# Kernel optimization log

Measured on AMD Instinct MI355X. Metric: run time of the kernel, lower is better.

The kernel has to match this reference:

```python
import jax, jax.numpy as jnp
import numpy as np

N = 30000      # nodes
NNZ = 480000   # edges (avg degree 16)
D_IN, D_H, D_OUT = 64, 256, 128


def spmm(rows, cols, vals, feat, n):
    # (sparse [n,n] in COO) @ feat : out[r] += vals[e] * feat[cols[e]]
    return jax.ops.segment_sum(vals[:, None] * feat[cols], rows, num_segments=n)


def graph_inception(l_feat, r_feat, rows, cols, vals, W1, b1, W2, b2):
    # hop=1, eval mode (F.dropout with training=False is identity)
    n = l_feat.shape[0]
    x0 = r_feat  # dropout(Korder_list[r][0])
    x1 = l_feat  # dropout(Korder_list[l][0])
    # network_l @ x0 and network_r (=transpose) @ x1
    l_K = spmm(rows, cols, vals, x0, n)          # [N, D]
    r_K = spmm(cols, rows, vals, x1, n)          # [N, D]
    l_re = l_K @ W1 + b1                          # weight1(l_Korder)
    r_re = r_K @ W1 + b1
    # Multiply: mm(network, a) * b then weight2 (mm result equals l_K / r_K)
    l_mul = (l_K * x1) @ W2 + b2
    r_mul = (r_K * x0) @ W2 + b2
    return l_re + l_mul, r_re + r_mul


def setup_inputs() -> dict:
    key = jax.random.key(0)
    ks = jax.random.split(key, 9)
    l_feat = jax.random.normal(ks[0], (N, D_IN), jnp.float32)
    r_feat = jax.random.normal(ks[1], (N, D_IN), jnp.float32)
    edge_rows = jax.random.randint(ks[2], (NNZ,), 0, N, jnp.int32)
    edge_cols = jax.random.randint(ks[3], (NNZ,), 0, N, jnp.int32)
    edge_vals = jax.random.uniform(ks[4], (NNZ,), jnp.float32)
    W1 = jax.random.normal(ks[5], (D_IN, D_H), jnp.float32) / np.sqrt(D_IN)
    W2 = jax.random.normal(ks[6], (D_IN, D_H), jnp.float32) / np.sqrt(D_IN)
    W3 = jax.random.normal(ks[7], (D_H, D_OUT), jnp.float32) / np.sqrt(D_H)
    W4 = jax.random.normal(ks[8], (D_H, D_OUT), jnp.float32) / np.sqrt(D_H)
    return {
        "l_feat": l_feat, "r_feat": r_feat,
        "edge_rows": edge_rows, "edge_cols": edge_cols, "edge_vals": edge_vals,
        "W1": W1, "b1": jnp.zeros((D_H,), jnp.float32),
        "W2": W2, "b2": jnp.zeros((D_H,), jnp.float32),
        "W3": W3, "b3": jnp.zeros((D_OUT,), jnp.float32),
        "W4": W4, "b4": jnp.zeros((D_OUT,), jnp.float32),
    }


def reference(l_feat, r_feat, edge_rows, edge_cols, edge_vals,
              W1, b1, W2, b2, W3, b3, W4, b4):
    a1, b1_ = graph_inception(l_feat, r_feat, edge_rows, edge_cols, edge_vals, W1, b1, W2, b2)
    y1 = jax.nn.relu(a1)
    z1 = jax.nn.relu(b1_)
    a2, _ = graph_inception(y1, z1, edge_rows, edge_cols, edge_vals, W3, b3, W4, b4)
    return jax.nn.relu(a2)  # [N, 128]
```

## Files before the change

### kernel.cpp

```cpp
#include <hip/hip_runtime.h>

#define NN     30000
#define NNZE   480000
#define NPART  8
#define PROWS  (NN / NPART)
#define NCHUNK 32
#define CH_E   (NNZE / NCHUNK)
#define QBIN   7500
#define SCB    118

using s8 = __attribute__((ext_vector_type(8))) short;
using f4 = __attribute__((ext_vector_type(4))) float;

__device__ __forceinline__ unsigned short f2bf(float x) {
    unsigned int u = __float_as_uint(x);
    u += 0x7fff + ((u >> 16) & 1);
    return (unsigned short)(u >> 16);
}
__device__ __forceinline__ float bf2f(unsigned short h) {
    return __uint_as_float(((unsigned int)h) << 16);
}
__device__ __forceinline__ float bflo(unsigned int z) {
    return __uint_as_float(z << 16);
}
__device__ __forceinline__ float bfhi(unsigned int z) {
    return __uint_as_float(z & 0xffff0000u);
}
__device__ __forceinline__ int2 nt_pair(const int2* p) {
    long long v = __builtin_nontemporal_load((const long long*)p);
    int2 r; r.x = (int)(unsigned int)v; r.y = (int)(v >> 32); return r;
}
__device__ __forceinline__ unsigned long long nt_u64(const void* p) {
    return __builtin_nontemporal_load((const unsigned long long*)p);
}

#define FEAT4   (NN * 64 / 4)
#define PREP_W0 (2 * FEAT4)
#define PREP_W1 (PREP_W0 + 98688)
__global__ __launch_bounds__(256) void prep_kernel(
    const float* __restrict__ lf, const float* __restrict__ rf,
    const float* __restrict__ W1, const float* __restrict__ W2,
    const float* __restrict__ W3, const float* __restrict__ W4,
    const float* __restrict__ b1, const float* __restrict__ b2,
    const float* __restrict__ b3, const float* __restrict__ b4,
    unsigned short* __restrict__ lfb, unsigned short* __restrict__ rfb,
    unsigned short* __restrict__ Wt1, unsigned short* __restrict__ Wt2,
    float* __restrict__ bias1, float* __restrict__ bias2)
{
    int i = blockIdx.x * 256 + threadIdx.x;
    if (i < PREP_W0) {
        const float* src = (i < FEAT4) ? lf : rf;
        unsigned short* dst = (i < FEAT4) ? lfb : rfb;
        int j = (i < FEAT4) ? i : i - FEAT4;
        float4 v = ((const float4*)src)[j];
        ushort4 o;
        o.x = f2bf(v.x); o.y = f2bf(v.y); o.z = f2bf(v.z); o.w = f2bf(v.w);
        ((ushort4*)dst)[j] = o;
    } else if (i < PREP_W1) {
        int j = i - PREP_W0;
        if (j < 32768) {
            int n = j >> 7, k = j & 127;
            float v = (k < 64) ? W1[(size_t)k * 256 + n] : W2[(size_t)(k - 64) * 256 + n];
            Wt1[j] = f2bf(v);
        } else if (j < 32768 + 65536) {
            int q = j - 32768;
            int n = q >> 9, k = q & 511;
            float v = (k < 256) ? W3[(size_t)k * 128 + n] : W4[(size_t)(k - 256) * 128 + n];
            Wt2[q] = f2bf(v);
        } else if (j < 98304 + 256) {
            int n = j - 98304; bias1[n] = b1[n] + b2[n];
        } else if (j < 98560 + 128) {
            int n = j - 98560; bias2[n] = b3[n] + b4[n];
        }
    }
}

__global__ __launch_bounds__(256) void count_rank_kernel(
    const int* __restrict__ rows, const int* __restrict__ cols,
    int* __restrict__ histP,
    unsigned short* __restrict__ rank_r, unsigned short* __restrict__ rank_c)
{
    int b = blockIdx.x;
    int side    = b >> 7;
    int chunk   = (b & 127) >> 2;
    int quarter = b & 3;
    const int* keys = side ? cols : rows;
    unsigned short* rank = side ? rank_c : rank_r;
    int binlo = quarter * QBIN;

    __shared__ int h[QBIN];
    for (int i = threadIdx.x; i < QBIN; i += 256) h[i] = 0;
    __syncthreads();

    int e0 = chunk * CH_E;
    for (int e = e0 + threadIdx.x; e < e0 + CH_E; e += 256) {
        int k = __builtin_nontemporal_load(keys + e) - binlo;
        if ((unsigned)k < (unsigned)QBIN)
            rank[e] = (unsigned short)atomicAdd(&h[k], 1);
    }
    __syncthreads();

    int* dst = histP + ((size_t)(side * NCHUNK + chunk)) * NN + binlo;
    for (int i = threadIdx.x; i < QBIN; i += 256)
        __builtin_nontemporal_store(h[i], dst + i);
}

__global__ __launch_bounds__(256) void scanP_kernel(
    int* __restrict__ histP,
    int* __restrict__ rp, int* __restrict__ cp, int* __restrict__ totals)
{
    int b = blockIdx.x;
    int side = (b >= SCB) ? 1 : 0;
    int lb = side ? b - SCB : b;
    int t = threadIdx.x;
    int bin = lb * 256 + t;

    int run = 0;
    if (bin < NN) {
        int* base = histP + (size_t)side * NCHUNK * NN + bin;
#pragma unroll 4
        for (int c = 0; c < NCHUNK; ++c) {
            int v = base[(size_t)c * NN];
            base[(size_t)c * NN] = run;
            run += v;
        }
    }
    __shared__ int s[256];
    s[t] = run;
    __syncthreads();
#pragma unroll
    for (int off = 1; off < 256; off <<= 1) {
        int u = (t >= off) ? s[t - off] : 0;
        __syncthreads();
        s[t] += u;
        __syncthreads();
    }
    if (bin < NN) (side ? cp : rp)[bin] = s[t] - run;
    if (t == 255) totals[b] = s[t];
}

__global__ __launch_bounds__(256) void scan_addtot_kernel(
    int* __restrict__ rp, int* __restrict__ cp, const int* __restrict__ totals)
{
    int b = blockIdx.x;
    int side = (b >= SCB) ? 1 : 0;
    int lb = side ? b - SCB : b;
    int t = threadIdx.x;

    __shared__ int s[128];
    if (t < 128) s[t] = (t < SCB) ? totals[side * SCB + t] : 0;
    __syncthreads();
#pragma unroll
    for (int off = 1; off < 128; off <<= 1) {
        int u = 0;
        if (t < 128 && t >= off) u = s[t - off];
        __syncthreads();
        if (t < 128) s[t] += u;
        __syncthreads();
    }
    int off = (lb == 0) ? 0 : s[lb - 1];
    int idx = lb * 256 + t;
    int* ptr = side ? cp : rp;
    if (idx < NN) ptr[idx] += off;
    if (b == 0   && t == 0) rp[NN] = NNZE;
    if (b == SCB && t == 0) cp[NN] = NNZE;
}

__global__ __launch_bounds__(256) void scatter_rank_kernel(
    const int* __restrict__ rows, const int* __restrict__ cols,
    const float* __restrict__ vals,
    const unsigned short* __restrict__ rank_r, const unsigned short* __restrict__ rank_c,
    const int* __restrict__ histP,
    const int* __restrict__ rp, const int* __restrict__ cp,
    int2* __restrict__ csr_pair, int2* __restrict__ csc_pair)
{
    int part = blockIdx.x & (NPART - 1);
    int lo = part * PROWS, hi = lo + PROWS;
    int nb = gridDim.x >> 3;
    int bj = blockIdx.x >> 3;
    int stride = nb * 256;
    for (int e = bj * 256 + threadIdx.x; e < NNZE; e += stride) {
        int r = __builtin_nontemporal_load(rows + e);
        int c = __builtin_nontemporal_load(cols + e);
        float fv = __builtin_nontemporal_load(vals + e);
        int vb = __float_as_int(fv);
        int chunk = e / CH_E;
        if (r >= lo && r < hi) {
            int p = rp[r] + histP[(size_t)chunk * NN + r]
                  + (int)__builtin_nontemporal_load(rank_r + e);
            csr_pair[p] = make_int2(c, vb);
        }
        if (c >= lo && c < hi) {
            int q = cp[c] + histP[(size_t)(NCHUNK + chunk) * NN + c]
                  + (int)__builtin_nontemporal_load(rank_c + e);
            csc_pair[q] = make_int2(r, vb);
        }
    }
}

#define G64CAP 768
__global__ __launch_bounds__(256) void gather64_x_kernel(
    const int* __restrict__ rp, const int2* __restrict__ rpair,
    const int* __restrict__ cp, const int2* __restrict__ cpair,
    const unsigned short* __restrict__ lfb, const unsigned short* __restrict__ rfb,
    unsigned short* __restrict__ X1, unsigned short* __restrict__ X2)
{
    int side = blockIdx.y;
    const int*  ptr  = side ? cp    : rp;
    const int2* pair = side ? cpair : rpair;
    const unsigned int* gf = (const unsigned int*)(side ? lfb : rfb);
    const unsigned int* mf = (const unsigned int*)(side ? rfb : lfb);
    unsigned int* X = (unsigned int*)(side ? X2 : X1);

    __shared__ int2 sp[G64CAP];
    int w0 = blockIdx.x * 8;
    int e0b = ptr[w0];
    int nseg = ptr[w0 + 8] - e0b;
    for (int i = threadIdx.x; i < nseg && i < G64CAP; i += 256)
        sp[i] = nt_pair(&pair[e0b + i]);
    __syncthreads();

    int w = w0 + (threadIdx.x >> 5);
    int l = threadIdx.x & 31;
    int ea = ptr[w] - e0b, eb = ptr[w + 1] - e0b;
    float a0 = 0.f, a1 = 0.f;
    int e = ea;
    for (; e + 7 < eb; e += 8) {
        int2 p[8];
#pragma unroll
        for (int j = 0; j < 8; ++j)
            p[j] = (e + j < G64CAP) ? sp[e + j] : nt_pair(&pair[e0b + e + j]);
        unsigned int z[8];
#pragma unroll
        for (int j = 0; j < 8; ++j) z[j] = gf[(size_t)p[j].x * 32 + l];
#pragma unroll
        for (int j = 0; j < 8; ++j) {
            float v = __int_as_float(p[j].y);
            a0 += v * bflo(z[j]);
            a1 += v * bfhi(z[j]);
        }
    }
    for (; e < eb; ++e) {
        int2 p0 = (e < G64CAP) ? sp[e] : nt_pair(&pair[e0b + e]);
        unsigned int z0 = gf[(size_t)p0.x * 32 + l];
        float v = __int_as_float(p0.y);
        a0 += v * bflo(z0);
        a1 += v * bfhi(z0);
    }
    unsigned int m = mf[(size_t)w * 32 + l];
    float m0 = a0 * bflo(m);
    float m1 = a1 * bfhi(m);
    unsigned int o0 = (unsigned int)f2bf(a0) | ((unsigned int)f2bf(a1) << 16);
    unsigned int o1 = (unsigned int)f2bf(m0) | ((unsigned int)f2bf(m1) << 16);
    __builtin_nontemporal_store(o0, &X[(size_t)w * 64 + l]);
    __builtin_nontemporal_store(o1, &X[(size_t)w * 64 + 32 + l]);
}

__global__ __launch_bounds__(256) void gather256_x_kernel(
    const int* __restrict__ ptr, const int2* __restrict__ pair,
    const unsigned short* __restrict__ z1b, const unsigned short* __restrict__ y1b,
    unsigned short* __restrict__ X3)
{
    int w    = blockIdx.x * 4 + (threadIdx.x >> 6);
    int lane = threadIdx.x & 63;
    int e0 = ptr[w], e1 = ptr[w + 1];
    const ushort4* Z = (const ushort4*)z1b;
    f4 acc = {0.f, 0.f, 0.f, 0.f};
    int e = e0;
    for (; e + 15 < e1; e += 16) {
        int2 p[16];
#pragma unroll
        for (int j = 0; j < 16; ++j) p[j] = nt_pair(&pair[e + j]);
        ushort4 z[16];
#pragma unroll
        for (int j = 0; j < 16; ++j) z[j] = Z[(size_t)p[j].x * 64 + lane];
#pragma unroll
        for (int j = 0; j < 16; ++j) {
            float v = __int_as_float(p[j].y);
            acc[0] += v * bf2f(z[j].x);
            acc[1] += v * bf2f(z[j].y);
            acc[2] += v * bf2f(z[j].z);
            acc[3] += v * bf2f(z[j].w);
        }
    }
    for (; e + 3 < e1; e += 4) {
        int2 p[4];
#pragma unroll
        for (int j = 0; j < 4; ++j) p[j] = nt_pair(&pair[e + j]);
        ushort4 z[4];
#pragma unroll
        for (int j = 0; j < 4; ++j) z[j] = Z[(size_t)p[j].x * 64 + lane];
#pragma unroll
        for (int j = 0; j < 4; ++j) {
            float v = __int_as_float(p[j].y);
            acc[0] += v * bf2f(z[j].x);
            acc[1] += v * bf2f(z[j].y);
            acc[2] += v * bf2f(z[j].z);
            acc[3] += v * bf2f(z[j].w);
        }
    }
    for (; e < e1; ++e) {
        int2 p0 = nt_pair(&pair[e]);
        float v0 = __int_as_float(p0.y);
        ushort4 z0 = Z[(size_t)p0.x * 64 + lane];
        acc[0] += v0 * bf2f(z0.x);
        acc[1] += v0 * bf2f(z0.y);
        acc[2] += v0 * bf2f(z0.z);
        acc[3] += v0 * bf2f(z0.w);
    }
    unsigned long long yu = nt_u64(&((const ushort4*)y1b)[(size_t)w * 64 + lane]);
    float y0 = bf2f((unsigned short)(yu));
    float y1 = bf2f((unsigned short)(yu >> 16));
    float y2 = bf2f((unsigned short)(yu >> 32));
    float y3 = bf2f((unsigned short)(yu >> 48));
    unsigned long long o0 =
        (unsigned long long)f2bf(acc[0])
      | ((unsigned long long)f2bf(acc[1]) << 16)
      | ((unsigned long long)f2bf(acc[2]) << 32)
      | ((unsigned long long)f2bf(acc[3]) << 48);
    unsigned long long o1 =
        (unsigned long long)f2bf(acc[0] * y0)
      | ((unsigned long long)f2bf(acc[1] * y1) << 16)
      | ((unsigned long long)f2bf(acc[2] * y2) << 32)
      | ((unsigned long long)f2bf(acc[3] * y3) << 48);
    unsigned long long* X3u = (unsigned long long*)X3;
    __builtin_nontemporal_store(o0, &X3u[(size_t)w * 128 + lane]);
    __builtin_nontemporal_store(o1, &X3u[(size_t)w * 128 + 64 + lane]);
}

template<int K, int DOUT, bool OUT_BF16, bool NT_A, bool NT_B>
__global__ __launch_bounds__(256) void mfma_gemm_kernel(
    const unsigned short* Xa, const unsigned short* Xb,
    const unsigned short* __restrict__ Wt, const float* __restrict__ bias,
    void* outa, void* outb)
{
    constexpr int WC = DOUT / 4;
    constexpr int FN = WC / 16;
    __shared__ s8 sX[64 * 8];
    __shared__ s8 sW[DOUT * 8];

    const unsigned short* X = blockIdx.y ? Xb : Xa;
    void* outv              = blockIdx.y ? outb : outa;
    const bool nt_out       = blockIdx.y ? NT_B : NT_A;

    const int t       = threadIdx.x;
    const int rowbase = blockIdx.x * 64;
    const int wid     = t >> 6;
    const int lane    = t & 63;
    const int l15     = lane & 15;
    const int kg      = lane >> 4;

    f4 acc[4][FN] = {};

    for (int kc = 0; kc < K; kc += 64) {
#pragma unroll
        for (int it = 0; it < 2; ++it) {
            int ch = t + it * 256;
            int r = ch >> 3, c = ch & 7;
            int row = rowbase + r;
            s8 v = {};
            if (row < NN)
                v = __builtin_nontemporal_load(((const s8*)X) + ((size_t)row * K + kc) / 8 + c);
            sX[(r << 3) | (c ^ (r & 7))] = v;
        }
#pragma unroll
        for (int it = 0; it < DOUT / 32; ++it) {
            int ch = t + it * 256;
            int n = ch >> 3, c = ch & 7;
            sW[(n << 3) | (c ^ (n & 7))] = ((const s8*)Wt)[((size_t)n * K + kc) / 8 + c];
        }
        __syncthreads();

#pragma unroll
        for (int ks = 0; ks < 2; ++ks) {
            int cch = ks * 4 + kg;
            s8 a[4], b[FN];
#pragma unroll
            for (int fm = 0; fm < 4; ++fm) {
                int r0 = fm * 16 + l15;
                a[fm] = sX[(r0 << 3) | (cch ^ (r0 & 7))];
            }
#pragma unroll
            for (int fn = 0; fn < FN; ++fn) {
                int n0 = wid * WC + fn * 16 + l15;
                b[fn] = sW[(n0 << 3) | (cch ^ (n0 & 7))];
            }
#pragma unroll
            for (int fm = 0; fm < 4; ++fm)
#pragma unroll
                for (int fn = 0; fn < FN; ++fn)
                    acc[fm][fn] = __builtin_amdgcn_mfma_f32_16x16x32_bf16(
                        a[fm], b[fn], acc[fm][fn], 0, 0, 0);
        }
        __syncthreads();
    }

#pragma unroll
    for (int fm = 0; fm < 4; ++fm) {
#pragma unroll
        for (int fn = 0; fn < FN; ++fn) {
            int col = wid * WC + fn * 16 + l15;
            float bv = bias[col];
#pragma unroll
            for (int j = 0; j < 4; ++j) {
                int row = rowbase + fm * 16 + kg * 4 + j;
                if (row < NN) {
                    float v = fmaxf(acc[fm][fn][j] + bv, 0.f);
                    if constexpr (OUT_BF16) {
                        unsigned short* q = (unsigned short*)outv + (size_t)row * DOUT + col;
                        if (nt_out) __builtin_nontemporal_store(f2bf(v), q);
                        else        *q = f2bf(v);
                    } else {
                        float* q = (float*)outv + (size_t)row * DOUT + col;
                        if (nt_out) __builtin_nontemporal_store(v, q);
                        else        *q = v;
                    }
                }
            }
        }
    }
}

extern "C" void kernel_launch(void* const* d_in, const int* in_sizes, int n_in,
                              void* d_out, int out_size, void* d_ws, size_t ws_size,
                              hipStream_t stream)
{
    const float* l_feat = (const float*)d_in[0];
    const float* r_feat = (const float*)d_in[1];
    const int*   rows   = (const int*)  d_in[2];
    const int*   cols   = (const int*)  d_in[3];
    const float* vals   = (const float*)d_in[4];
    const float* W1     = (const float*)d_in[5];
    const float* b1     = (const float*)d_in[6];
    const float* W2     = (const float*)d_in[7];
    const float* b2     = (const float*)d_in[8];
    const float* W3     = (const float*)d_in[9];
    const float* b3     = (const float*)d_in[10];
    const float* W4     = (const float*)d_in[11];
    const float* b4     = (const float*)d_in[12];
    float* out = (float*)d_out;

    char* p = (char*)d_ws;
    unsigned short* X1  = (unsigned short*)p; p += (size_t)NN * 128 * 2;
    unsigned short* X2  = (unsigned short*)p; p += (size_t)NN * 128 * 2;
    unsigned short* X3  = (unsigned short*)p; p += (size_t)NN * 512 * 2;
    unsigned short* z1b = (unsigned short*)p; p += (size_t)NN * 256 * 2;
    unsigned short* y1b = (unsigned short*)p; p += (size_t)NN * 256 * 2;
    unsigned short* lfb = (unsigned short*)p; p += (size_t)NN * 64 * 2;
    unsigned short* rfb = (unsigned short*)p; p += (size_t)NN * 64 * 2;
    int* histP    = (int*)p; p += (size_t)2 * NCHUNK * NN * 4;
    int* totals   = (int*)p; p += 256 * 4;
    unsigned short* Wt1 = (unsigned short*)p; p += 32768 * 2;
    unsigned short* Wt2 = (unsigned short*)p; p += 65536 * 2;
    float* bias1 = (float*)p; p += 256 * 4;
    float* bias2 = (float*)p; p += 128 * 4;
    int*   row_ptr  = (int*)p; p += (size_t)(NN + 4) * 4;
    int*   col_ptr  = (int*)p; p += (size_t)(NN + 4) * 4;
    int2*  csr_pair = (int2*)p; p += (size_t)NNZE * 8;
    int2*  csc_pair = (int2*)p; p += (size_t)NNZE * 8;
    unsigned short* rank_r = (unsigned short*)p; p += (size_t)NNZE * 2;
    unsigned short* rank_c = (unsigned short*)p; p += (size_t)NNZE * 2;

    prep_kernel<<<(PREP_W1 + 255) / 256, 256, 0, stream>>>(
        l_feat, r_feat, W1, W2, W3, W4, b1, b2, b3, b4,
        lfb, rfb, Wt1, Wt2, bias1, bias2);

    count_rank_kernel<<<256, 256, 0, stream>>>(rows, cols, histP, rank_r, rank_c);

    scanP_kernel<<<2 * SCB, 256, 0, stream>>>(histP, row_ptr, col_ptr, totals);
    scan_addtot_kernel<<<2 * SCB, 256, 0, stream>>>(row_ptr, col_ptr, totals);

    scatter_rank_kernel<<<2048, 256, 0, stream>>>(
        rows, cols, vals, rank_r, rank_c, histP, row_ptr, col_ptr, csr_pair, csc_pair);

    {
        dim3 grid(NN / 8, 2);
        gather64_x_kernel<<<grid, 256, 0, stream>>>(
            row_ptr, csr_pair, col_ptr, csc_pair, lfb, rfb, X1, X2);
    }

    {
        dim3 grid((NN + 63) / 64, 2);
        mfma_gemm_kernel<128, 256, true, true, false><<<grid, 256, 0, stream>>>(
            X1, X2, Wt1, bias1, y1b, z1b);
    }

    gather256_x_kernel<<<NN / 4, 256, 0, stream>>>(row_ptr, csr_pair, z1b, y1b, X3);

    {
        dim3 grid((NN + 63) / 64, 1);
        mfma_gemm_kernel<512, 128, false, true, true><<<grid, 256, 0, stream>>>(
            X3, X3, Wt2, bias2, out, out);
    }
}
```

Baseline: 200.3 us.

## Pack CSR edges into 32-bit index+bf16 value, merge prep with counting

Edge entries are packed as a 15-bit node index plus a bf16 edge value in one 32-bit word, halving CSR/CSC storage and gather-side index traffic. The prep and histogram-count kernels are fused into one launch, and the 256-wide gather is reworked to 32 lanes per row loading 8 bf16 values each. This risks precision loss from rounding edge values to bf16. The 15-bit index mask holds only because N=30000 fits in 32768.

New measurement: 200.8 us. About the same (+0.2%).

```diff
diff --git a/kernel.cpp b/kernel.cpp
--- a/kernel.cpp
+++ b/kernel.cpp
@@ -26,18 +26,19 @@
 __device__ __forceinline__ float bfhi(unsigned int z) {
     return __uint_as_float(z & 0xffff0000u);
 }
-__device__ __forceinline__ int2 nt_pair(const int2* p) {
-    long long v = __builtin_nontemporal_load((const long long*)p);
-    int2 r; r.x = (int)(unsigned int)v; r.y = (int)(v >> 32); return r;
-}
-__device__ __forceinline__ unsigned long long nt_u64(const void* p) {
-    return __builtin_nontemporal_load((const unsigned long long*)p);
+__device__ __forceinline__ int nt_i32(const int* p) {
+    return __builtin_nontemporal_load(p);
+}
+
+__device__ __forceinline__ unsigned int pack_iv(int idx, float v) {
+    return (unsigned int)(idx & 0x7fff) | ((unsigned int)f2bf(v) << 16);
 }
 
 #define FEAT4   (NN * 64 / 4)
 #define PREP_W0 (2 * FEAT4)
 #define PREP_W1 (PREP_W0 + 98688)
-__global__ __launch_bounds__(256) void prep_kernel(
+#define PREPB   ((PREP_W1 + 255) / 256)
+__global__ __launch_bounds__(256) void prep_count_kernel(
     const float* __restrict__ lf, const float* __restrict__ rf,
     const float* __restrict__ W1, const float* __restrict__ W2,
     const float* __restrict__ W3, const float* __restrict__ W4,
@@ -45,42 +46,44 @@
     const float* __restrict__ b3, const float* __restrict__ b4,
     unsigned short* __restrict__ lfb, unsigned short* __restrict__ rfb,
     unsigned short* __restrict__ Wt1, unsigned short* __restrict__ Wt2,
-    float* __restrict__ bias1, float* __restrict__ bias2)
-{
-    int i = blockIdx.x * 256 + threadIdx.x;
-    if (i < PREP_W0) {
-        const float* src = (i < FEAT4) ? lf : rf;
-        unsigned short* dst = (i < FEAT4) ? lfb : rfb;
-        int j = (i < FEAT4) ? i : i - FEAT4;
-        float4 v = ((const float4*)src)[j];
-        ushort4 o;
-        o.x = f2bf(v.x); o.y = f2bf(v.y); o.z = f2bf(v.z); o.w = f2bf(v.w);
-        ((ushort4*)dst)[j] = o;
-    } else if (i < PREP_W1) {
-        int j = i - PREP_W0;
-        if (j < 32768) {
-            int n = j >> 7, k = j & 127;
-            float v = (k < 64) ? W1[(size_t)k * 256 + n] : W2[(size_t)(k - 64) * 256 + n];
-            Wt1[j] = f2bf(v);
-        } else if (j < 32768 + 65536) {
-            int q = j - 32768;
-            int n = q >> 9, k = q & 511;
-            float v = (k < 256) ? W3[(size_t)k * 128 + n] : W4[(size_t)(k - 256) * 128 + n];
-            Wt2[q] = f2bf(v);
-        } else if (j < 98304 + 256) {
-            int n = j - 98304; bias1[n] = b1[n] + b2[n];
-        } else if (j < 98560 + 128) {
-            int n = j - 98560; bias2[n] = b3[n] + b4[n];
-        }
-    }
-}
-
-__global__ __launch_bounds__(256) void count_rank_kernel(
+    float* __restrict__ bias1, float* __restrict__ bias2,
     const int* __restrict__ rows, const int* __restrict__ cols,
     int* __restrict__ histP,
     unsigned short* __restrict__ rank_r, unsigned short* __restrict__ rank_c)
 {
-    int b = blockIdx.x;
+    __shared__ int h[QBIN];
+
+    if (blockIdx.x < PREPB) {
+        int i = blockIdx.x * 256 + threadIdx.x;
+        if (i < PREP_W0) {
+            const float* src = (i < FEAT4) ? lf : rf;
+            unsigned short* dst = (i < FEAT4) ? lfb : rfb;
+            int j = (i < FEAT4) ? i : i - FEAT4;
+            float4 v = ((const float4*)src)[j];
+            ushort4 o;
+            o.x = f2bf(v.x); o.y = f2bf(v.y); o.z = f2bf(v.z); o.w = f2bf(v.w);
+            ((ushort4*)dst)[j] = o;
+        } else if (i < PREP_W1) {
+            int j = i - PREP_W0;
+            if (j < 32768) {
+                int n = j >> 7, k = j & 127;
+                float v = (k < 64) ? W1[(size_t)k * 256 + n] : W2[(size_t)(k - 64) * 256 + n];
+                Wt1[j] = f2bf(v);
+            } else if (j < 32768 + 65536) {
+                int q = j - 32768;
+                int n = q >> 9, k = q & 511;
+                float v = (k < 256) ? W3[(size_t)k * 128 + n] : W4[(size_t)(k - 256) * 128 + n];
+                Wt2[q] = f2bf(v);
+            } else if (j < 98304 + 256) {
+                int n = j - 98304; bias1[n] = b1[n] + b2[n];
+            } else if (j < 98560 + 128) {
+                int n = j - 98560; bias2[n] = b3[n] + b4[n];
+            }
+        }
+        return;
+    }
+
+    int b = blockIdx.x - PREPB;
     int side    = b >> 7;
     int chunk   = (b & 127) >> 2;
     int quarter = b & 3;
@@ -88,13 +91,12 @@
     unsigned short* rank = side ? rank_c : rank_r;
     int binlo = quarter * QBIN;
 
-    __shared__ int h[QBIN];
     for (int i = threadIdx.x; i < QBIN; i += 256) h[i] = 0;
     __syncthreads();
 
     int e0 = chunk * CH_E;
     for (int e = e0 + threadIdx.x; e < e0 + CH_E; e += 256) {
-        int k = __builtin_nontemporal_load(keys + e) - binlo;
+        int k = nt_i32(keys + e) - binlo;
         if ((unsigned)k < (unsigned)QBIN)
             rank[e] = (unsigned short)atomicAdd(&h[k], 1);
     }
@@ -172,7 +174,7 @@
     const unsigned short* __restrict__ rank_r, const unsigned short* __restrict__ rank_c,
     const int* __restrict__ histP,
     const int* __restrict__ rp, const int* __restrict__ cp,
-    int2* __restrict__ csr_pair, int2* __restrict__ csc_pair)
+    unsigned int* __restrict__ csr_pw, unsigned int* __restrict__ csc_pw)
 {
     int part = blockIdx.x & (NPART - 1);
     int lo = part * PROWS, hi = lo + PROWS;
@@ -180,44 +182,43 @@
     int bj = blockIdx.x >> 3;
     int stride = nb * 256;
     for (int e = bj * 256 + threadIdx.x; e < NNZE; e += stride) {
-        int r = __builtin_nontemporal_load(rows + e);
-        int c = __builtin_nontemporal_load(cols + e);
+        int r = nt_i32(rows + e);
+        int c = nt_i32(cols + e);
         float fv = __builtin_nontemporal_load(vals + e);
-        int vb = __float_as_int(fv);
         int chunk = e / CH_E;
         if (r >= lo && r < hi) {
             int p = rp[r] + histP[(size_t)chunk * NN + r]
                   + (int)__builtin_nontemporal_load(rank_r + e);
-            csr_pair[p] = make_int2(c, vb);
+            csr_pw[p] = pack_iv(c, fv);
         }
         if (c >= lo && c < hi) {
             int q = cp[c] + histP[(size_t)(NCHUNK + chunk) * NN + c]
                   + (int)__builtin_nontemporal_load(rank_c + e);
-            csc_pair[q] = make_int2(r, vb);
+            csc_pw[q] = pack_iv(r, fv);
         }
     }
 }
 
 #define G64CAP 768
 __global__ __launch_bounds__(256) void gather64_x_kernel(
-    const int* __restrict__ rp, const int2* __restrict__ rpair,
-    const int* __restrict__ cp, const int2* __restrict__ cpair,
+    const int* __restrict__ rp, const unsigned int* __restrict__ rpw,
+    const int* __restrict__ cp, const unsigned int* __restrict__ cpw,
     const unsigned short* __restrict__ lfb, const unsigned short* __restrict__ rfb,
     unsigned short* __restrict__ X1, unsigned short* __restrict__ X2)
 {
     int side = blockIdx.y;
-    const int*  ptr  = side ? cp    : rp;
-    const int2* pair = side ? cpair : rpair;
+    const int*          ptr = side ? cp  : rp;
+    const unsigned int* pw  = side ? cpw : rpw;
     const unsigned int* gf = (const unsigned int*)(side ? lfb : rfb);
     const unsigned int* mf = (const unsigned int*)(side ? rfb : lfb);
     unsigned int* X = (unsigned int*)(side ? X2 : X1);
 
-    __shared__ int2 sp[G64CAP];
+    __shared__ unsigned int sp[G64CAP];
     int w0 = blockIdx.x * 8;
     int e0b = ptr[w0];
     int nseg = ptr[w0 + 8] - e0b;
     for (int i = threadIdx.x; i < nseg && i < G64CAP; i += 256)
-        sp[i] = nt_pair(&pair[e0b + i]);
+        sp[i] = __builtin_nontemporal_load(pw + e0b + i);
     __syncthreads();
 
     int w = w0 + (threadIdx.x >> 5);
@@ -226,24 +227,26 @@
     float a0 = 0.f, a1 = 0.f;
     int e = ea;
     for (; e + 7 < eb; e += 8) {
-        int2 p[8];
+        unsigned int p[8];
 #pragma unroll
         for (int j = 0; j < 8; ++j)
-            p[j] = (e + j < G64CAP) ? sp[e + j] : nt_pair(&pair[e0b + e + j]);
+            p[j] = (e + j < G64CAP) ? sp[e + j]
+                                    : __builtin_nontemporal_load(pw + e0b + e + j);
         unsigned int z[8];
 #pragma unroll
-        for (int j = 0; j < 8; ++j) z[j] = gf[(size_t)p[j].x * 32 + l];
+        for (int j = 0; j < 8; ++j) z[j] = gf[(size_t)(p[j] & 0x7fff) * 32 + l];
 #pragma unroll
         for (int j = 0; j < 8; ++j) {
-            float v = __int_as_float(p[j].y);
+            float v = bfhi(p[j]);
             a0 += v * bflo(z[j]);
             a1 += v * bfhi(z[j]);
         }
     }
     for (; e < eb; ++e) {
-        int2 p0 = (e < G64CAP) ? sp[e] : nt_pair(&pair[e0b + e]);
-        unsigned int z0 = gf[(size_t)p0.x * 32 + l];
-        float v = __int_as_float(p0.y);
+        unsigned int p0 = (e < G64CAP) ? sp[e]
+                                       : __builtin_nontemporal_load(pw + e0b + e);
+        unsigned int z0 = gf[(size_t)(p0 & 0x7fff) * 32 + l];
+        float v = bfhi(p0);
         a0 += v * bflo(z0);
         a1 += v * bfhi(z0);
     }
@@ -257,75 +260,49 @@
 }
 
 __global__ __launch_bounds__(256) void gather256_x_kernel(
-    const int* __restrict__ ptr, const int2* __restrict__ pair,
+    const int* __restrict__ ptr, const unsigned int* __restrict__ pw,
     const unsigned short* __restrict__ z1b, const unsigned short* __restrict__ y1b,
     unsigned short* __restrict__ X3)
 {
-    int w    = blockIdx.x * 4 + (threadIdx.x >> 6);
-    int lane = threadIdx.x & 63;
+    int w = blockIdx.x * 8 + (threadIdx.x >> 5);
+    int l = threadIdx.x & 31;
     int e0 = ptr[w], e1 = ptr[w + 1];
-    const ushort4* Z = (const ushort4*)z1b;
-    f4 acc = {0.f, 0.f, 0.f, 0.f};
+    const s8* Z = (const s8*)z1b;
+    float acc[8] = {};
     int e = e0;
-    for (; e + 15 < e1; e += 16) {
-        int2 p[16];
-#pragma unroll
-        for (int j = 0; j < 16; ++j) p[j] = nt_pair(&pair[e + j]);
-        ushort4 z[16];
-#pragma unroll
-        for (int j = 0; j < 16; ++j) z[j] = Z[(size_t)p[j].x * 64 + lane];
-#pragma unroll
-        for (int j = 0; j < 16; ++j) {
-            float v = __int_as_float(p[j].y);
-            acc[0] += v * bf2f(z[j].x);
-            acc[1] += v * bf2f(z[j].y);
-            acc[2] += v * bf2f(z[j].z);
-            acc[3] += v * bf2f(z[j].w);
-        }
-    }
-    for (; e + 3 < e1; e += 4) {
-        int2 p[4];
-#pragma unroll
-        for (int j = 0; j < 4; ++j) p[j] = nt_pair(&pair[e + j]);
-        ushort4 z[4];
-#pragma unroll
-        for (int j = 0; j < 4; ++j) z[j] = Z[(size_t)p[j].x * 64 + lane];
-#pragma unroll
-        for (int j = 0; j < 4; ++j) {
-            float v = __int_as_float(p[j].y);
-            acc[0] += v * bf2f(z[j].x);
-            acc[1] += v * bf2f(z[j].y);
-            acc[2] += v * bf2f(z[j].z);
-            acc[3] += v * bf2f(z[j].w);
+    for (; e + 7 < e1; e += 8) {
+        unsigned int p[8];
+#pragma unroll
+        for (int j = 0; j < 8; ++j) p[j] = __builtin_nontemporal_load(pw + e + j);
+        s8 z[8];
+#pragma unroll
+        for (int j = 0; j < 8; ++j) z[j] = Z[(size_t)(p[j] & 0x7fff) * 32 + l];
+#pragma unroll
+        for (int j = 0; j < 8; ++j) {
+            float v = bfhi(p[j]);
+#pragma unroll
+            for (int q = 0; q < 8; ++q)
+                acc[q] += v * bf2f((unsigned short)z[j][q]);
         }
     }
     for (; e < e1; ++e) {
-        int2 p0 = nt_pair(&pair[e]);
-        float v0 = __int_as_float(p0.y);
-        ushort4 z0 = Z[(size_t)p0.x * 64 + lane];
-        acc[0] += v0 * bf2f(z0.x);
-        acc[1] += v0 * bf2f(z0.y);
-        acc[2] += v0 * bf2f(z0.z);
-        acc[3] += v0 * bf2f(z0.w);
-    }
-    unsigned long long yu = nt_u64(&((const ushort4*)y1b)[(size_t)w * 64 + lane]);
-    float y0 = bf2f((unsigned short)(yu));
-    float y1 = bf2f((unsigned short)(yu >> 16));
-    float y2 = bf2f((unsigned short)(yu >> 32));
-    float y3 = bf2f((unsigned short)(yu >> 48));
-    unsigned long long o0 =
-        (unsigned long long)f2bf(acc[0])
-      | ((unsigned long long)f2bf(acc[1]) << 16)
-      | ((unsigned long long)f2bf(acc[2]) << 32)
-      | ((unsigned long long)f2bf(acc[3]) << 48);
-    unsigned long long o1 =
-        (unsigned long long)f2bf(acc[0] * y0)
-      | ((unsigned long long)f2bf(acc[1] * y1) << 16)
-      | ((unsigned long long)f2bf(acc[2] * y2) << 32)
-      | ((unsigned long long)f2bf(acc[3] * y3) << 48);
-    unsigned long long* X3u = (unsigned long long*)X3;
-    __builtin_nontemporal_store(o0, &X3u[(size_t)w * 128 + lane]);
-    __builtin_nontemporal_store(o1, &X3u[(size_t)w * 128 + 64 + lane]);
+        unsigned int p0 = __builtin_nontemporal_load(pw + e);
+        float v = bfhi(p0);
+        s8 z0 = Z[(size_t)(p0 & 0x7fff) * 32 + l];
+#pragma unroll
+        for (int q = 0; q < 8; ++q)
+            acc[q] += v * bf2f((unsigned short)z0[q]);
+    }
+    s8 yv = ((const s8*)y1b)[(size_t)w * 32 + l];
+    s8 o0, o1;
+#pragma unroll
+    for (int q = 0; q < 8; ++q) {
+        o0[q] = (short)f2bf(acc[q]);
+        o1[q] = (short)f2bf(acc[q] * bf2f((unsigned short)yv[q]));
+    }
+    s8* X3v = (s8*)X3;
+    __builtin_nontemporal_store(o0, &X3v[(size_t)w * 64 + l]);
+    __builtin_nontemporal_store(o1, &X3v[(size_t)w * 64 + 32 + l]);
 }
 
 template<int K, int DOUT, bool OUT_BF16, bool NT_A, bool NT_B>
@@ -456,27 +433,26 @@
     float* bias2 = (float*)p; p += 128 * 4;
     int*   row_ptr  = (int*)p; p += (size_t)(NN + 4) * 4;
     int*   col_ptr  = (int*)p; p += (size_t)(NN + 4) * 4;
-    int2*  csr_pair = (int2*)p; p += (size_t)NNZE * 8;
-    int2*  csc_pair = (int2*)p; p += (size_t)NNZE * 8;
+    unsigned int* csr_pw = (unsigned int*)p; p += (size_t)NNZE * 4;
+    unsigned int* csc_pw = (unsigned int*)p; p += (size_t)NNZE * 4;
     unsigned short* rank_r = (unsigned short*)p; p += (size_t)NNZE * 2;
     unsigned short* rank_c = (unsigned short*)p; p += (size_t)NNZE * 2;
 
-    prep_kernel<<<(PREP_W1 + 255) / 256, 256, 0, stream>>>(
+    prep_count_kernel<<<PREPB + 256, 256, 0, stream>>>(
         l_feat, r_feat, W1, W2, W3, W4, b1, b2, b3, b4,
-        lfb, rfb, Wt1, Wt2, bias1, bias2);
-
-    count_rank_kernel<<<256, 256, 0, stream>>>(rows, cols, histP, rank_r, rank_c);
+        lfb, rfb, Wt1, Wt2, bias1, bias2,
+        rows, cols, histP, rank_r, rank_c);
 
     scanP_kernel<<<2 * SCB, 256, 0, stream>>>(histP, row_ptr, col_ptr, totals);
     scan_addtot_kernel<<<2 * SCB, 256, 0, stream>>>(row_ptr, col_ptr, totals);
 
     scatter_rank_kernel<<<2048, 256, 0, stream>>>(
-        rows, cols, vals, rank_r, rank_c, histP, row_ptr, col_ptr, csr_pair, csc_pair);
+        rows, cols, vals, rank_r, rank_c, histP, row_ptr, col_ptr, csr_pw, csc_pw);
 
     {
         dim3 grid(NN / 8, 2);
         gather64_x_kernel<<<grid, 256, 0, stream>>>(
-            row_ptr, csr_pair, col_ptr, csc_pair, lfb, rfb, X1, X2);
+            row_ptr, csr_pw, col_ptr, csc_pw, lfb, rfb, X1, X2);
     }
 
     {
@@ -485,7 +461,7 @@
             X1, X2, Wt1, bias1, y1b, z1b);
     }
 
-    gather256_x_kernel<<<NN / 4, 256, 0, stream>>>(row_ptr, csr_pair, z1b, y1b, X3);
+    gather256_x_kernel<<<NN / 8, 256, 0, stream>>>(row_ptr, csr_pw, z1b, y1b, X3);
 
     {
         dim3 grid((NN + 63) / 64, 1);
```
